# Optimization experiments

Measured on AMD Instinct MI355X. Metric: run time of the kernel, lower is better.

The kernel has to match this reference:

```python
import jax, jax.numpy as jnp
import numpy as np

B = 1024
IN_FEATURES = 4096
OUT_FEATURES = 4096
TOP_K = 64  # both k_prev (input width) and output top_k in this config


def setup_inputs() -> dict:
    key = jax.random.key(0)
    k1, k2, k3, k4 = jax.random.split(key, 4)
    bound = 1.0 / np.sqrt(IN_FEATURES)
    return {
        "input": jax.random.normal(k1, (B, TOP_K), dtype=jnp.float32),
        "weight": jax.random.uniform(k2, (OUT_FEATURES, IN_FEATURES), dtype=jnp.float32, minval=-bound, maxval=bound),
        "bias": jax.random.uniform(k3, (OUT_FEATURES,), dtype=jnp.float32, minval=-bound, maxval=bound),
        "previously_selected_nodes": jax.random.randint(k4, (B, TOP_K), 0, IN_FEATURES, dtype=jnp.int64).astype(jnp.int32),
    }


def reference(input, weight, bias, previously_selected_nodes):
    # Gather selected input-dim columns of weight per sample:
    # weight: (O, I), idx: (B, K) -> w_sel: (B, K, O)
    w_sel = jnp.take(weight.T, previously_selected_nodes, axis=0)
    # Batched matvec: (B, K, O) x (B, K) -> (B, O), plus bias
    result = jnp.einsum("bko,bk->bo", w_sel, input) + bias
    # Top-k selection over out_features, keep values and indices
    values, selected_nodes = jax.lax.top_k(result, TOP_K)
    return values, selected_nodes
```

## Files before the change

kernel.cpp:

```cpp
#include <hip/hip_runtime.h>
#include <stdint.h>

#define B_N 1024
#define K_N 64
#define O_N 4096
#define I_N 4096

typedef float nvec4 __attribute__((ext_vector_type(4)));

__global__ __launch_bounds__(256) void xpose_small(
    const float* __restrict__ x, const float* __restrict__ idxf,
    float* __restrict__ xT, float* __restrict__ idxTf) {
  __shared__ float tile[64][65];
  const int t = threadIdx.x;
  const int which = blockIdx.x >> 4;
  const int b0 = (blockIdx.x & 15) * 64;
  const float* src = which ? idxf : x;
  float* dst = which ? idxTf : xT;
  {
    const int r = t & 63;
    const int q0 = t >> 6;
#pragma unroll
    for (int jj = 0; jj < 4; ++jj) {
      const int q = q0 + 4 * jj;
      const float4 v = *(const float4*)(src + (size_t)(b0 + r) * K_N + 4 * q);
      tile[r][4 * q + 0] = v.x;
      tile[r][4 * q + 1] = v.y;
      tile[r][4 * q + 2] = v.z;
      tile[r][4 * q + 3] = v.w;
    }
  }
  __syncthreads();
  {
    const int kk = t & 63;
    const int q0 = t >> 6;
#pragma unroll
    for (int jj = 0; jj < 4; ++jj) {
      const int qb = q0 + 4 * jj;
      float4 v;
      v.x = tile[4 * qb + 0][kk];
      v.y = tile[4 * qb + 1][kk];
      v.z = tile[4 * qb + 2][kk];
      v.w = tile[4 * qb + 3][kk];
      *(float4*)(dst + (size_t)kk * B_N + b0 + 4 * qb) = v;
    }
  }
}

#define GEMV_COMPUTE(G)                                                   \
  do {                                                                    \
    const int o0 = (G)*8;                                                 \
    const int b = t;                                                      \
    const float4 bvA = *(const float4*)(bias + o0);                       \
    const float4 bvB = *(const float4*)(bias + o0 + 4);                   \
    float4 aA = make_float4(0.f, 0.f, 0.f, 0.f);                          \
    float4 aB = make_float4(0.f, 0.f, 0.f, 0.f);                          \
    float xr[4];                                                          \
    int ir[4];                                                            \
    _Pragma("unroll") for (int d = 0; d < 4; ++d) {                       \
      xr[d] = xT[d * B_N + b];                                            \
      ir[d] = idxT[d * B_N + b];                                          \
    }                                                                     \
    _Pragma("unroll") for (int k = 0; k < K_N; ++k) {                     \
      const float xk = xr[k & 3];                                         \
      const int i = ir[k & 3];                                            \
      if (k + 4 < K_N) {                                                  \
        xr[k & 3] = xT[(k + 4) * B_N + b];                                \
        ir[k & 3] = idxT[(k + 4) * B_N + b];                              \
      }                                                                   \
      const float4 wA = Wi[i];                                            \
      const float4 wB = Wi[I_N + i];                                      \
      aA.x = __fadd_rn(aA.x, __fmul_rn(xk, wA.x));                        \
      aA.y = __fadd_rn(aA.y, __fmul_rn(xk, wA.y));                        \
      aA.z = __fadd_rn(aA.z, __fmul_rn(xk, wA.z));                        \
      aA.w = __fadd_rn(aA.w, __fmul_rn(xk, wA.w));                        \
      aB.x = __fadd_rn(aB.x, __fmul_rn(xk, wB.x));                        \
      aB.y = __fadd_rn(aB.y, __fmul_rn(xk, wB.y));                        \
      aB.z = __fadd_rn(aB.z, __fmul_rn(xk, wB.z));                        \
      aB.w = __fadd_rn(aB.w, __fmul_rn(xk, wB.w));                        \
    }                                                                     \
    aA.x = __fadd_rn(aA.x, bvA.x);                                        \
    aA.y = __fadd_rn(aA.y, bvA.y);                                        \
    aA.z = __fadd_rn(aA.z, bvA.z);                                        \
    aA.w = __fadd_rn(aA.w, bvA.w);                                        \
    aB.x = __fadd_rn(aB.x, bvB.x);                                        \
    aB.y = __fadd_rn(aB.y, bvB.y);                                        \
    aB.z = __fadd_rn(aB.z, bvB.z);                                        \
    aB.w = __fadd_rn(aB.w, bvB.w);                                        \
    *(float4*)(res + (size_t)b * O_N + o0) = aA;                          \
    *(float4*)(res + (size_t)b * O_N + o0 + 4) = aB;                      \
  } while (0)

__global__ __launch_bounds__(1024, 4) void gemv_lds8(
    const float* __restrict__ W, const float* __restrict__ xT,
    const int* __restrict__ idxT, const float* __restrict__ bias,
    float* __restrict__ res) {
  __shared__ float4 Wi[2 * I_N];
  const int t = threadIdx.x;
  const int i0 = 4 * t;
  const int xcd = blockIdx.x & 7;
  const int jj = blockIdx.x >> 3;
  const int g0 = (xcd * 32 + jj) * 2;

  nvec4 r0, r1, r2, r3, r4, r5, r6, r7;
  {
    const float* Wp = W + (size_t)g0 * 8 * I_N + i0;
    r0 = __builtin_nontemporal_load((const nvec4*)(Wp + 0 * (size_t)I_N));
    r1 = __builtin_nontemporal_load((const nvec4*)(Wp + 1 * (size_t)I_N));
    r2 = __builtin_nontemporal_load((const nvec4*)(Wp + 2 * (size_t)I_N));
    r3 = __builtin_nontemporal_load((const nvec4*)(Wp + 3 * (size_t)I_N));
    r4 = __builtin_nontemporal_load((const nvec4*)(Wp + 4 * (size_t)I_N));
    r5 = __builtin_nontemporal_load((const nvec4*)(Wp + 5 * (size_t)I_N));
    r6 = __builtin_nontemporal_load((const nvec4*)(Wp + 6 * (size_t)I_N));
    r7 = __builtin_nontemporal_load((const nvec4*)(Wp + 7 * (size_t)I_N));
  }
  Wi[i0 + 0] = make_float4(r0.x, r1.x, r2.x, r3.x);
  Wi[i0 + 1] = make_float4(r0.y, r1.y, r2.y, r3.y);
  Wi[i0 + 2] = make_float4(r0.z, r1.z, r2.z, r3.z);
  Wi[i0 + 3] = make_float4(r0.w, r1.w, r2.w, r3.w);
  Wi[I_N + i0 + 0] = make_float4(r4.x, r5.x, r6.x, r7.x);
  Wi[I_N + i0 + 1] = make_float4(r4.y, r5.y, r6.y, r7.y);
  Wi[I_N + i0 + 2] = make_float4(r4.z, r5.z, r6.z, r7.z);
  Wi[I_N + i0 + 3] = make_float4(r4.w, r5.w, r6.w, r7.w);
  {
    const float* Wp = W + ((size_t)g0 + 1) * 8 * I_N + i0;
    r0 = __builtin_nontemporal_load((const nvec4*)(Wp + 0 * (size_t)I_N));
    r1 = __builtin_nontemporal_load((const nvec4*)(Wp + 1 * (size_t)I_N));
    r2 = __builtin_nontemporal_load((const nvec4*)(Wp + 2 * (size_t)I_N));
    r3 = __builtin_nontemporal_load((const nvec4*)(Wp + 3 * (size_t)I_N));
    r4 = __builtin_nontemporal_load((const nvec4*)(Wp + 4 * (size_t)I_N));
    r5 = __builtin_nontemporal_load((const nvec4*)(Wp + 5 * (size_t)I_N));
    r6 = __builtin_nontemporal_load((const nvec4*)(Wp + 6 * (size_t)I_N));
    r7 = __builtin_nontemporal_load((const nvec4*)(Wp + 7 * (size_t)I_N));
  }
  __syncthreads();

  GEMV_COMPUTE(g0);

  __syncthreads();
  Wi[i0 + 0] = make_float4(r0.x, r1.x, r2.x, r3.x);
  Wi[i0 + 1] = make_float4(r0.y, r1.y, r2.y, r3.y);
  Wi[i0 + 2] = make_float4(r0.z, r1.z, r2.z, r3.z);
  Wi[i0 + 3] = make_float4(r0.w, r1.w, r2.w, r3.w);
  Wi[I_N + i0 + 0] = make_float4(r4.x, r5.x, r6.x, r7.x);
  Wi[I_N + i0 + 1] = make_float4(r4.y, r5.y, r6.y, r7.y);
  Wi[I_N + i0 + 2] = make_float4(r4.z, r5.z, r6.z, r7.z);
  Wi[I_N + i0 + 3] = make_float4(r4.w, r5.w, r6.w, r7.w);
  __syncthreads();

  GEMV_COMPUTE(g0 + 1);
}

#define H16S 260
__global__ __launch_bounds__(256) void topk_phase(
    const float* __restrict__ res, float* __restrict__ out) {
  __shared__ __align__(16) unsigned int hist[256];
  __shared__ __align__(16) unsigned int hist16[16 * H16S];
  __shared__ unsigned int sel_u[64];
  __shared__ int sel_i[64];
  __shared__ int eqlist[128];
  __shared__ unsigned int s_cntgt, s_cnteq;
  __shared__ unsigned int s_remaining, s_prefix;

  const int t = threadIdx.x;
  const int b = blockIdx.x;

  hist[t] = 0u;
#pragma unroll
  for (int j = 0; j < 17; ++j) {
    const int z = t + 256 * j;
    if (z < 16 * H16S) hist16[z] = 0u;
  }
  if (t == 0) {
    s_remaining = 64u;
    s_prefix = 0u;
    s_cntgt = 0u;
    s_cnteq = 0u;
  }

  unsigned int myu[16];
#pragma unroll
  for (int jf = 0; jf < 4; ++jf) {
    const float4 v =
        *(const float4*)(res + (size_t)b * O_N + 1024 * jf + 4 * t);
    const float fv[4] = {v.x, v.y, v.z, v.w};
#pragma unroll
    for (int c = 0; c < 4; ++c) {
      const unsigned int s = __float_as_uint(fv[c]);
      myu[jf * 4 + c] = (s & 0x80000000u) ? ~s : (s | 0x80000000u);
    }
  }
  __syncthreads();

  for (int round = 3; round >= 0; --round) {
    const int shift = round * 8;
    const unsigned int pfx = s_prefix;
    const unsigned int rem = s_remaining;
    if (round == 3) {
      const int rep = (t & 15) * H16S;
#pragma unroll
      for (int j = 0; j < 16; ++j)
        atomicAdd(&hist16[rep + (myu[j] >> 24)], 1u);
    } else {
      const unsigned int himask = 0xFFFFFFFFu << (shift + 8);
#pragma unroll
      for (int j = 0; j < 16; ++j) {
        if ((myu[j] & himask) == (pfx & himask))
          atomicAdd(&hist[(myu[j] >> shift) & 255u], 1u);
      }
    }
    __syncthreads();
    if (t < 64) {
      uint4 h;
      if (round == 3) {
        h = make_uint4(0u, 0u, 0u, 0u);
#pragma unroll
        for (int r = 0; r < 16; ++r) {
          const uint4 hh = *(const uint4*)&hist16[r * H16S + 4 * t];
          h.x += hh.x;
          h.y += hh.y;
          h.z += hh.z;
          h.w += hh.w;
        }
      } else {
        h = *(const uint4*)&hist[4 * t];
      }
      unsigned int s0 = h.x + h.y + h.z + h.w;
      unsigned int run = s0;
#pragma unroll
      for (int off = 1; off < 64; off <<= 1) {
        const unsigned int v = __shfl_down(run, off, 64);
        if (t + off < 64) run += v;
      }
      const unsigned int above = run - s0;
      unsigned int cge[4], cgt[4];
      cgt[3] = above;
      cge[3] = above + h.w;
      cgt[2] = cge[3];
      cge[2] = cge[3] + h.z;
      cgt[1] = cge[2];
      cge[1] = cge[2] + h.y;
      cgt[0] = cge[1];
      cge[0] = cge[1] + h.x;
#pragma unroll
      for (int j = 0; j < 4; ++j) {
        if (cge[j] >= rem && cgt[j] < rem) {
          s_prefix = pfx | ((unsigned int)(4 * t + j) << shift);
          s_remaining = rem - cgt[j];
        }
      }
      *(uint4*)&hist[4 * t] = make_uint4(0u, 0u, 0u, 0u);
    }
    __syncthreads();
  }
  const unsigned int ustar = s_prefix;

#pragma unroll
  for (int j = 0; j < 16; ++j) {
    const unsigned int u = myu[j];
    const int oi = 4 * t + (j & 3) + 1024 * (j >> 2);
    if (u > ustar) {
      unsigned int p = atomicAdd(&s_cntgt, 1u);
      sel_u[p] = u;
      sel_i[p] = oi;
    } else if (u == ustar) {
      unsigned int p = atomicAdd(&s_cnteq, 1u);
      if (p < 128u) eqlist[p] = oi;
    }
  }
  __syncthreads();

  if (t == 0 && s_cnteq > 1u) {
    int n = (int)(s_cnteq < 128u ? s_cnteq : 128u);
    for (int a = 1; a < n; ++a) {
      int v = eqlist[a];
      int c = a;
      while (c > 0 && eqlist[c - 1] > v) {
        eqlist[c] = eqlist[c - 1];
        --c;
      }
      eqlist[c] = v;
    }
  }
  __syncthreads();

  if (t < 64) {
    const int n_gt = (int)s_cntgt;
    unsigned int u;
    int oi;
    if (t < n_gt) {
      u = sel_u[t];
      oi = sel_i[t];
    } else {
      u = ustar;
      oi = eqlist[t - n_gt];
    }
    unsigned long long key =
        ((unsigned long long)(~u) << 32) | (unsigned int)oi;
    for (int kk = 2; kk <= 64; kk <<= 1) {
      for (int jj = kk >> 1; jj > 0; jj >>= 1) {
        unsigned long long partner = __shfl_xor(key, jj, 64);
        const bool up = ((t & kk) == 0);
        const bool lower = ((t & jj) == 0);
        unsigned long long mn = key < partner ? key : partner;
        unsigned long long mx = key < partner ? partner : key;
        key = (up == lower) ? mn : mx;
      }
    }
    const unsigned int su = ~(unsigned int)(key >> 32);
    const int so = (int)(key & 0xFFFFFFFFu);
    const float f = (su & 0x80000000u) ? __uint_as_float(su ^ 0x80000000u)
                                       : __uint_as_float(~su);
    out[b * 64 + t] = f;
    out[B_N * 64 + b * 64 + t] = (float)so;
  }
}

__global__ __launch_bounds__(256) void selgemv_topk(
    const float* __restrict__ x, const float* __restrict__ Wsrc,
    const float* __restrict__ bias, const int* __restrict__ idx,
    float* __restrict__ out) {
  __shared__ float sx[K_N];
  __shared__ int si[K_N];
  __shared__ float svals[O_N];
  __shared__ unsigned int hist[256];
  __shared__ unsigned int scan[256];
  __shared__ unsigned int sel_u[64];
  __shared__ int sel_i[64];
  __shared__ int eqlist[128];
  __shared__ unsigned int s_T, s_ngt, s_cntgt, s_cnteq;
  __shared__ unsigned int s_remaining, s_prefix;

  const int t = threadIdx.x;
  const int b = blockIdx.x;

  if (t < K_N) {
    sx[t] = x[b * K_N + t];
    si[t] = idx[b * K_N + t];
  }
  if (t == 0) {
    s_remaining = 64u;
    s_prefix = 0u;
    s_cntgt = 0u;
    s_cnteq = 0u;
  }
  __syncthreads();

  float acc[16];
#pragma unroll
  for (int j = 0; j < 16; ++j) acc[j] = 0.0f;

  for (int k = 0; k < K_N; ++k) {
    const float xk = sx[k];
    const int ik = si[k];
#pragma unroll
    for (int j = 0; j < 4; ++j) {
      int o0 = (j * 256 + t) * 4;
#pragma unroll
      for (int c = 0; c < 4; ++c) {
        float w = Wsrc[(size_t)(o0 + c) * I_N + ik];
        acc[4 * j + c] = __fadd_rn(acc[4 * j + c], __fmul_rn(xk, w));
      }
    }
  }

#pragma unroll
  for (int j = 0; j < 4; ++j) {
    int g = j * 256 + t;
    float4 bb = ((const float4*)bias)[g];
    float4 r;
    r.x = __fadd_rn(acc[4 * j + 0], bb.x);
    r.y = __fadd_rn(acc[4 * j + 1], bb.y);
    r.z = __fadd_rn(acc[4 * j + 2], bb.z);
    r.w = __fadd_rn(acc[4 * j + 3], bb.w);
    ((float4*)svals)[g] = r;
  }
  __syncthreads();

  unsigned int myu[16];
#pragma unroll
  for (int j = 0; j < 16; ++j) {
    float f = svals[t + 256 * j];
    unsigned int s = __float_as_uint(f);
    myu[j] = (s & 0x80000000u) ? ~s : (s | 0x80000000u);
  }

  for (int round = 3; round >= 0; --round) {
    const int shift = round * 8;
    hist[t] = 0u;
    __syncthreads();
    const unsigned int pfx = s_prefix;
    const unsigned int rem = s_remaining;
    const unsigned int himask =
        (round == 3) ? 0u : (0xFFFFFFFFu << (shift + 8));
#pragma unroll
    for (int j = 0; j < 16; ++j) {
      if ((myu[j] & himask) == (pfx & himask))
        atomicAdd(&hist[(myu[j] >> shift) & 255u], 1u);
    }
    __syncthreads();
    scan[t] = hist[t];
    __syncthreads();
    for (int off = 1; off < 256; off <<= 1) {
      unsigned int v = (t + off < 256) ? scan[t + off] : 0u;
      __syncthreads();
      scan[t] += v;
      __syncthreads();
    }
    const unsigned int c_ge = scan[t];
    const unsigned int c_gt = (t < 255) ? scan[t + 1] : 0u;
    if (c_ge >= rem && c_gt < rem) {
      s_T = (unsigned int)t;
      s_ngt = c_gt;
    }
    __syncthreads();
    if (t == 0) {
      s_prefix |= (s_T << shift);
      s_remaining -= s_ngt;
    }
    __syncthreads();
  }
  const unsigned int ustar = s_prefix;

#pragma unroll
  for (int j = 0; j < 16; ++j) {
    const unsigned int u = myu[j];
    if (u > ustar) {
      unsigned int p = atomicAdd(&s_cntgt, 1u);
      sel_u[p] = u;
      sel_i[p] = t + 256 * j;
    } else if (u == ustar) {
      unsigned int p = atomicAdd(&s_cnteq, 1u);
      if (p < 128u) eqlist[p] = t + 256 * j;
    }
  }
  __syncthreads();

  if (t == 0 && s_cnteq > 1u) {
    int n = (int)(s_cnteq < 128u ? s_cnteq : 128u);
    for (int a = 1; a < n; ++a) {
      int v = eqlist[a];
      int c = a;
      while (c > 0 && eqlist[c - 1] > v) {
        eqlist[c] = eqlist[c - 1];
        --c;
      }
      eqlist[c] = v;
    }
  }
  __syncthreads();

  if (t < 64) {
    const int n_gt = (int)s_cntgt;
    unsigned int u;
    int oi;
    if (t < n_gt) {
      u = sel_u[t];
      oi = sel_i[t];
    } else {
      u = ustar;
      oi = eqlist[t - n_gt];
    }
    unsigned long long key =
        ((unsigned long long)(~u) << 32) | (unsigned int)oi;
    for (int kk = 2; kk <= 64; kk <<= 1) {
      for (int jj = kk >> 1; jj > 0; jj >>= 1) {
        unsigned long long partner = __shfl_xor(key, jj, 64);
        const bool up = ((t & kk) == 0);
        const bool lower = ((t & jj) == 0);
        unsigned long long mn = key < partner ? key : partner;
        unsigned long long mx = key < partner ? partner : key;
        key = (up == lower) ? mn : mx;
      }
    }
    const unsigned int su = ~(unsigned int)(key >> 32);
    const int so = (int)(key & 0xFFFFFFFFu);
    const float f = (su & 0x80000000u) ? __uint_as_float(su ^ 0x80000000u)
                                       : __uint_as_float(~su);
    out[b * 64 + t] = f;
    out[B_N * 64 + b * 64 + t] = (float)so;
  }
}

extern "C" void kernel_launch(void* const* d_in, const int* in_sizes, int n_in,
                              void* d_out, int out_size, void* d_ws,
                              size_t ws_size, hipStream_t stream) {
  const float* x = (const float*)d_in[0];
  const float* W = (const float*)d_in[1];
  const float* bias = (const float*)d_in[2];
  const int* idx = (const int*)d_in[3];
  float* out = (float*)d_out;

  const size_t xT_bytes = (size_t)K_N * B_N * sizeof(float);
  const size_t idxT_bytes = xT_bytes;
  const size_t res_bytes = (size_t)B_N * O_N * sizeof(float);

  if (ws_size >= xT_bytes + idxT_bytes + res_bytes) {
    float* xT = (float*)d_ws;
    float* idxTf = (float*)((char*)d_ws + xT_bytes);
    float* res = (float*)((char*)d_ws + xT_bytes + idxT_bytes);
    xpose_small<<<32, 256, 0, stream>>>(x, (const float*)idx, xT, idxTf);
    gemv_lds8<<<256, 1024, 0, stream>>>(W, xT, (const int*)idxTf, bias, res);
    topk_phase<<<B_N, 256, 0, stream>>>(res, out);
  } else {
    selgemv_topk<<<B_N, 256, 0, stream>>>(x, W, bias, idx, out);
  }
}
```

Before: 148.6 us.

## Fuse transpose, gather-GEMV and top-k into one cooperative kernel with grid syncs

Replaces the three-kernel pipeline (transpose, GEMV, per-row top-k) with a single cooperative launch of 256 blocks of 1024 threads. Grid-wide syncs separate the phases, and the W prefetch overlaps the transpose done by the first 8 blocks. The top-k phase runs four 256-thread groups per block, with each group's scratch carved out of the reused LDS buffer. This removes launch gaps and tail effects between kernels, at the cost of grid-sync overhead and only one 1024-thread block per CU for the top-k phase, with the old path kept as a fallback if the cooperative launch fails.

```diff
diff --git a/kernel.cpp b/kernel.cpp
--- a/kernel.cpp
+++ b/kernel.cpp
@@ -1,51 +1,25 @@
 #include <hip/hip_runtime.h>
+#include <hip/hip_cooperative_groups.h>
 #include <stdint.h>
+
+namespace cg = cooperative_groups;
 
 #define B_N 1024
 #define K_N 64
 #define O_N 4096
 #define I_N 4096
+#define H16S 260
 
 typedef float nvec4 __attribute__((ext_vector_type(4)));
 
-__global__ __launch_bounds__(256) void xpose_small(
-    const float* __restrict__ x, const float* __restrict__ idxf,
-    float* __restrict__ xT, float* __restrict__ idxTf) {
-  __shared__ float tile[64][65];
-  const int t = threadIdx.x;
-  const int which = blockIdx.x >> 4;
-  const int b0 = (blockIdx.x & 15) * 64;
-  const float* src = which ? idxf : x;
-  float* dst = which ? idxTf : xT;
-  {
-    const int r = t & 63;
-    const int q0 = t >> 6;
-#pragma unroll
-    for (int jj = 0; jj < 4; ++jj) {
-      const int q = q0 + 4 * jj;
-      const float4 v = *(const float4*)(src + (size_t)(b0 + r) * K_N + 4 * q);
-      tile[r][4 * q + 0] = v.x;
-      tile[r][4 * q + 1] = v.y;
-      tile[r][4 * q + 2] = v.z;
-      tile[r][4 * q + 3] = v.w;
-    }
-  }
-  __syncthreads();
-  {
-    const int kk = t & 63;
-    const int q0 = t >> 6;
-#pragma unroll
-    for (int jj = 0; jj < 4; ++jj) {
-      const int qb = q0 + 4 * jj;
-      float4 v;
-      v.x = tile[4 * qb + 0][kk];
-      v.y = tile[4 * qb + 1][kk];
-      v.z = tile[4 * qb + 2][kk];
-      v.w = tile[4 * qb + 3][kk];
-      *(float4*)(dst + (size_t)kk * B_N + b0 + 4 * qb) = v;
-    }
-  }
-}
+struct TopkSh {
+  unsigned int hist[256];
+  unsigned int hist16[16 * H16S];
+  unsigned int sel_u[64];
+  int sel_i[64];
+  int eqlist[128];
+  unsigned int s_cntgt, s_cnteq, s_remaining, s_prefix;
+};
 
 #define GEMV_COMPUTE(G)                                                   \
   do {                                                                    \
@@ -91,16 +65,20 @@
     *(float4*)(res + (size_t)b * O_N + o0 + 4) = aB;                      \
   } while (0)
 
-__global__ __launch_bounds__(1024, 4) void gemv_lds8(
-    const float* __restrict__ W, const float* __restrict__ xT,
-    const int* __restrict__ idxT, const float* __restrict__ bias,
-    float* __restrict__ res) {
-  __shared__ float4 Wi[2 * I_N];
+__global__ __launch_bounds__(1024, 1) void fused_all(
+    const float* __restrict__ W, const float* __restrict__ x,
+    const float* __restrict__ idxf, const float* __restrict__ bias,
+    float* __restrict__ xT, float* __restrict__ idxTf,
+    float* __restrict__ res, float* __restrict__ out) {
+  __shared__ __align__(16) float4 Wi[2 * I_N];
+  cg::grid_group grid = cg::this_grid();
+
   const int t = threadIdx.x;
+  const int bx = blockIdx.x;
+  const int xcd = bx & 7;
+  const int jjb = bx >> 3;
+  const int g0 = (xcd * 32 + jjb) * 2;
   const int i0 = 4 * t;
-  const int xcd = blockIdx.x & 7;
-  const int jj = blockIdx.x >> 3;
-  const int g0 = (xcd * 32 + jj) * 2;
 
   nvec4 r0, r1, r2, r3, r4, r5, r6, r7;
   {
@@ -114,6 +92,42 @@
     r6 = __builtin_nontemporal_load((const nvec4*)(Wp + 6 * (size_t)I_N));
     r7 = __builtin_nontemporal_load((const nvec4*)(Wp + 7 * (size_t)I_N));
   }
+
+  if (bx < 8) {
+    float* tile = (float*)Wi;
+    for (int job = bx * 4; job < bx * 4 + 4; ++job) {
+      const int which = job >> 4;
+      const int b0 = (job & 15) * 64;
+      const float* src = which ? idxf : x;
+      float* dst = which ? idxTf : xT;
+      {
+        const int r = t & 63;
+        const int q = t >> 6;
+        const float4 v =
+            *(const float4*)(src + (size_t)(b0 + r) * K_N + 4 * q);
+        tile[r * 65 + 4 * q + 0] = v.x;
+        tile[r * 65 + 4 * q + 1] = v.y;
+        tile[r * 65 + 4 * q + 2] = v.z;
+        tile[r * 65 + 4 * q + 3] = v.w;
+      }
+      __syncthreads();
+      {
+        const int kk = t & 63;
+        const int qb = t >> 6;
+        float4 v;
+        v.x = tile[(4 * qb + 0) * 65 + kk];
+        v.y = tile[(4 * qb + 1) * 65 + kk];
+        v.z = tile[(4 * qb + 2) * 65 + kk];
+        v.w = tile[(4 * qb + 3) * 65 + kk];
+        *(float4*)(dst + (size_t)kk * B_N + b0 + 4 * qb) = v;
+      }
+      __syncthreads();
+    }
+  }
+
+  grid.sync();
+
+  const int* idxT = (const int*)idxTf;
   Wi[i0 + 0] = make_float4(r0.x, r1.x, r2.x, r3.x);
   Wi[i0 + 1] = make_float4(r0.y, r1.y, r2.y, r3.y);
   Wi[i0 + 2] = make_float4(r0.z, r1.z, r2.z, r3.z);
@@ -149,9 +163,266 @@
   __syncthreads();
 
   GEMV_COMPUTE(g0 + 1);
+
+  grid.sync();
+
+  {
+    const int g = t >> 8;
+    const int tl = t & 255;
+    const int row = bx * 4 + g;
+    TopkSh* sh = ((TopkSh*)Wi) + g;
+
+    sh->hist[tl] = 0u;
+#pragma unroll
+    for (int j = 0; j < 17; ++j) {
+      const int z = tl + 256 * j;
+      if (z < 16 * H16S) sh->hist16[z] = 0u;
+    }
+    if (tl == 0) {
+      sh->s_remaining = 64u;
+      sh->s_prefix = 0u;
+      sh->s_cntgt = 0u;
+      sh->s_cnteq = 0u;
+    }
+
+    unsigned int myu[16];
+#pragma unroll
+    for (int jf = 0; jf < 4; ++jf) {
+      const float4 v =
+          *(const float4*)(res + (size_t)row * O_N + 1024 * jf + 4 * tl);
+      const float fv[4] = {v.x, v.y, v.z, v.w};
+#pragma unroll
+      for (int c = 0; c < 4; ++c) {
+        const unsigned int s = __float_as_uint(fv[c]);
+        myu[jf * 4 + c] = (s & 0x80000000u) ? ~s : (s | 0x80000000u);
+      }
+    }
+    __syncthreads();
+
+    for (int round = 3; round >= 0; --round) {
+      const int shift = round * 8;
+      const unsigned int pfx = sh->s_prefix;
+      const unsigned int rem = sh->s_remaining;
+      if (round == 3) {
+        const int rep = (tl & 15) * H16S;
+#pragma unroll
+        for (int j = 0; j < 16; ++j)
+          atomicAdd(&sh->hist16[rep + (myu[j] >> 24)], 1u);
+      } else {
+        const unsigned int himask = 0xFFFFFFFFu << (shift + 8);
+#pragma unroll
+        for (int j = 0; j < 16; ++j) {
+          if ((myu[j] & himask) == (pfx & himask))
+            atomicAdd(&sh->hist[(myu[j] >> shift) & 255u], 1u);
+        }
+      }
+      __syncthreads();
+      if (tl < 64) {
+        uint4 h;
+        if (round == 3) {
+          h = make_uint4(0u, 0u, 0u, 0u);
+#pragma unroll
+          for (int r = 0; r < 16; ++r) {
+            const uint4 hh = *(const uint4*)&sh->hist16[r * H16S + 4 * tl];
+            h.x += hh.x;
+            h.y += hh.y;
+            h.z += hh.z;
+            h.w += hh.w;
+          }
+        } else {
+          h = *(const uint4*)&sh->hist[4 * tl];
+        }
+        unsigned int s0 = h.x + h.y + h.z + h.w;
+        unsigned int run = s0;
+#pragma unroll
+        for (int off = 1; off < 64; off <<= 1) {
+          const unsigned int v = __shfl_down(run, off, 64);
+          if (tl + off < 64) run += v;
+        }
+        const unsigned int above = run - s0;
+        unsigned int cge[4], cgt[4];
+        cgt[3] = above;
+        cge[3] = above + h.w;
+        cgt[2] = cge[3];
+        cge[2] = cge[3] + h.z;
+        cgt[1] = cge[2];
+        cge[1] = cge[2] + h.y;
+        cgt[0] = cge[1];
+        cge[0] = cge[1] + h.x;
+#pragma unroll
+        for (int j = 0; j < 4; ++j) {
+          if (cge[j] >= rem && cgt[j] < rem) {
+            sh->s_prefix = pfx | ((unsigned int)(4 * tl + j) << shift);
+            sh->s_remaining = rem - cgt[j];
+          }
+        }
+        *(uint4*)&sh->hist[4 * tl] = make_uint4(0u, 0u, 0u, 0u);
+      }
+      __syncthreads();
+    }
+    const unsigned int ustar = sh->s_prefix;
+
+#pragma unroll
+    for (int j = 0; j < 16; ++j) {
+      const unsigned int u = myu[j];
+      const int oi = 4 * tl + (j & 3) + 1024 * (j >> 2);
+      if (u > ustar) {
+        unsigned int p = atomicAdd(&sh->s_cntgt, 1u);
+        sh->sel_u[p] = u;
+        sh->sel_i[p] = oi;
+      } else if (u == ustar) {
+        unsigned int p = atomicAdd(&sh->s_cnteq, 1u);
+        if (p < 128u) sh->eqlist[p] = oi;
+      }
+    }
+    __syncthreads();
+
+    if (tl == 0 && sh->s_cnteq > 1u) {
+      int n = (int)(sh->s_cnteq < 128u ? sh->s_cnteq : 128u);
+      for (int a = 1; a < n; ++a) {
+        int v = sh->eqlist[a];
+        int c = a;
+        while (c > 0 && sh->eqlist[c - 1] > v) {
+          sh->eqlist[c] = sh->eqlist[c - 1];
+          --c;
+        }
+        sh->eqlist[c] = v;
+      }
+    }
+    __syncthreads();
+
+    if (tl < 64) {
+      const int n_gt = (int)sh->s_cntgt;
+      unsigned int u;
+      int oi;
+      if (tl < n_gt) {
+        u = sh->sel_u[tl];
+        oi = sh->sel_i[tl];
+      } else {
+        u = ustar;
+        oi = sh->eqlist[tl - n_gt];
+      }
+      unsigned long long key =
+          ((unsigned long long)(~u) << 32) | (unsigned int)oi;
+      for (int kk = 2; kk <= 64; kk <<= 1) {
+        for (int jj = kk >> 1; jj > 0; jj >>= 1) {
+          unsigned long long partner = __shfl_xor(key, jj, 64);
+          const bool up = ((tl & kk) == 0);
+          const bool lower = ((tl & jj) == 0);
+          unsigned long long mn = key < partner ? key : partner;
+          unsigned long long mx = key < partner ? partner : key;
+          key = (up == lower) ? mn : mx;
+        }
+      }
+      const unsigned int su = ~(unsigned int)(key >> 32);
+      const int so = (int)(key & 0xFFFFFFFFu);
+      const float f = (su & 0x80000000u) ? __uint_as_float(su ^ 0x80000000u)
+                                         : __uint_as_float(~su);
+      out[row * 64 + tl] = f;
+      out[B_N * 64 + row * 64 + tl] = (float)so;
+    }
+  }
 }
 
-#define H16S 260
+__global__ __launch_bounds__(256) void xpose_small(
+    const float* __restrict__ x, const float* __restrict__ idxf,
+    float* __restrict__ xT, float* __restrict__ idxTf) {
+  __shared__ float tile[64][65];
+  const int t = threadIdx.x;
+  const int which = blockIdx.x >> 4;
+  const int b0 = (blockIdx.x & 15) * 64;
+  const float* src = which ? idxf : x;
+  float* dst = which ? idxTf : xT;
+  {
+    const int r = t & 63;
+    const int q0 = t >> 6;
+#pragma unroll
+    for (int jj = 0; jj < 4; ++jj) {
+      const int q = q0 + 4 * jj;
+      const float4 v = *(const float4*)(src + (size_t)(b0 + r) * K_N + 4 * q);
+      tile[r][4 * q + 0] = v.x;
+      tile[r][4 * q + 1] = v.y;
+      tile[r][4 * q + 2] = v.z;
+      tile[r][4 * q + 3] = v.w;
+    }
+  }
+  __syncthreads();
+  {
+    const int kk = t & 63;
+    const int q0 = t >> 6;
+#pragma unroll
+    for (int jj = 0; jj < 4; ++jj) {
+      const int qb = q0 + 4 * jj;
+      float4 v;
+      v.x = tile[4 * qb + 0][kk];
+      v.y = tile[4 * qb + 1][kk];
+      v.z = tile[4 * qb + 2][kk];
+      v.w = tile[4 * qb + 3][kk];
+      *(float4*)(dst + (size_t)kk * B_N + b0 + 4 * qb) = v;
+    }
+  }
+}
+
+__global__ __launch_bounds__(1024, 4) void gemv_lds8(
+    const float* __restrict__ W, const float* __restrict__ xT,
+    const int* __restrict__ idxT, const float* __restrict__ bias,
+    float* __restrict__ res) {
+  __shared__ float4 Wi[2 * I_N];
+  const int t = threadIdx.x;
+  const int i0 = 4 * t;
+  const int xcd = blockIdx.x & 7;
+  const int jj = blockIdx.x >> 3;
+  const int g0 = (xcd * 32 + jj) * 2;
+
+  nvec4 r0, r1, r2, r3, r4, r5, r6, r7;
+  {
+    const float* Wp = W + (size_t)g0 * 8 * I_N + i0;
+    r0 = __builtin_nontemporal_load((const nvec4*)(Wp + 0 * (size_t)I_N));
+    r1 = __builtin_nontemporal_load((const nvec4*)(Wp + 1 * (size_t)I_N));
+    r2 = __builtin_nontemporal_load((const nvec4*)(Wp + 2 * (size_t)I_N));
+    r3 = __builtin_nontemporal_load((const nvec4*)(Wp + 3 * (size_t)I_N));
+    r4 = __builtin_nontemporal_load((const nvec4*)(Wp + 4 * (size_t)I_N));
+    r5 = __builtin_nontemporal_load((const nvec4*)(Wp + 5 * (size_t)I_N));
+    r6 = __builtin_nontemporal_load((const nvec4*)(Wp + 6 * (size_t)I_N));
+    r7 = __builtin_nontemporal_load((const nvec4*)(Wp + 7 * (size_t)I_N));
+  }
+  Wi[i0 + 0] = make_float4(r0.x, r1.x, r2.x, r3.x);
+  Wi[i0 + 1] = make_float4(r0.y, r1.y, r2.y, r3.y);
+  Wi[i0 + 2] = make_float4(r0.z, r1.z, r2.z, r3.z);
+  Wi[i0 + 3] = make_float4(r0.w, r1.w, r2.w, r3.w);
+  Wi[I_N + i0 + 0] = make_float4(r4.x, r5.x, r6.x, r7.x);
+  Wi[I_N + i0 + 1] = make_float4(r4.y, r5.y, r6.y, r7.y);
+  Wi[I_N + i0 + 2] = make_float4(r4.z, r5.z, r6.z, r7.z);
+  Wi[I_N + i0 + 3] = make_float4(r4.w, r5.w, r6.w, r7.w);
+  {
+    const float* Wp = W + ((size_t)g0 + 1) * 8 * I_N + i0;
+    r0 = __builtin_nontemporal_load((const nvec4*)(Wp + 0 * (size_t)I_N));
+    r1 = __builtin_nontemporal_load((const nvec4*)(Wp + 1 * (size_t)I_N));
+    r2 = __builtin_nontemporal_load((const nvec4*)(Wp + 2 * (size_t)I_N));
+    r3 = __builtin_nontemporal_load((const nvec4*)(Wp + 3 * (size_t)I_N));
+    r4 = __builtin_nontemporal_load((const nvec4*)(Wp + 4 * (size_t)I_N));
+    r5 = __builtin_nontemporal_load((const nvec4*)(Wp + 5 * (size_t)I_N));
+    r6 = __builtin_nontemporal_load((const nvec4*)(Wp + 6 * (size_t)I_N));
+    r7 = __builtin_nontemporal_load((const nvec4*)(Wp + 7 * (size_t)I_N));
+  }
+  __syncthreads();
+
+  GEMV_COMPUTE(g0);
+
+  __syncthreads();
+  Wi[i0 + 0] = make_float4(r0.x, r1.x, r2.x, r3.x);
+  Wi[i0 + 1] = make_float4(r0.y, r1.y, r2.y, r3.y);
+  Wi[i0 + 2] = make_float4(r0.z, r1.z, r2.z, r3.z);
+  Wi[i0 + 3] = make_float4(r0.w, r1.w, r2.w, r3.w);
+  Wi[I_N + i0 + 0] = make_float4(r4.x, r5.x, r6.x, r7.x);
+  Wi[I_N + i0 + 1] = make_float4(r4.y, r5.y, r6.y, r7.y);
+  Wi[I_N + i0 + 2] = make_float4(r4.z, r5.z, r6.z, r7.z);
+  Wi[I_N + i0 + 3] = make_float4(r4.w, r5.w, r6.w, r7.w);
+  __syncthreads();
+
+  GEMV_COMPUTE(g0 + 1);
+}
+
 __global__ __launch_bounds__(256) void topk_phase(
     const float* __restrict__ res, float* __restrict__ out) {
   __shared__ __align__(16) unsigned int hist[256];
@@ -499,9 +770,18 @@
     float* xT = (float*)d_ws;
     float* idxTf = (float*)((char*)d_ws + xT_bytes);
     float* res = (float*)((char*)d_ws + xT_bytes + idxT_bytes);
-    xpose_small<<<32, 256, 0, stream>>>(x, (const float*)idx, xT, idxTf);
-    gemv_lds8<<<256, 1024, 0, stream>>>(W, xT, (const int*)idxTf, bias, res);
-    topk_phase<<<B_N, 256, 0, stream>>>(res, out);
+
+    const float* idxf = (const float*)idx;
+    void* args[] = {(void*)&W,   (void*)&x,   (void*)&idxf, (void*)&bias,
+                    (void*)&xT,  (void*)&idxTf, (void*)&res, (void*)&out};
+    hipError_t e = hipLaunchCooperativeKernel(
+        (const void*)fused_all, dim3(256), dim3(1024), args, 0, stream);
+    if (e != hipSuccess) {
+      xpose_small<<<32, 256, 0, stream>>>(x, (const float*)idx, xT, idxTf);
+      gemv_lds8<<<O_N / 16, 1024, 0, stream>>>(W, xT, (const int*)idxTf,
+                                               bias, res);
+      topk_phase<<<B_N, 256, 0, stream>>>(res, out);
+    }
   } else {
     selgemv_topk<<<B_N, 256, 0, stream>>>(x, W, bias, idx, out);
   }
```

After: 497.4 us. 3.35x slower.
